# Kernel optimization log

Hardware: AMD Instinct MI355X
Metric: run time of the kernel (lower is better)

## Reference

```python
import jax, jax.numpy as jnp
import numpy as np

N = 6144
IN_FEATS = 512
OUT_FEATS = 64
NHEADS = 8
ALPHA = 0.2
NEG_BIG = -9e15


def setup_inputs() -> dict:
    key = jax.random.key(0)
    k_x, k_adj, k_w, k_a1, k_a2 = jax.random.split(key, 5)
    x = jax.random.normal(k_x, (N, IN_FEATS), dtype=jnp.float32)
    adj = jax.random.randint(k_adj, (N, N), 0, 2, dtype=jnp.int32)
    # xavier_uniform with gain=1.414 ~ sqrt(2)
    gain = 1.414
    bw = gain * np.sqrt(6.0 / (IN_FEATS + OUT_FEATS))
    W = jax.random.uniform(k_w, (NHEADS, IN_FEATS, OUT_FEATS), jnp.float32, -bw, bw)
    ba = gain * np.sqrt(6.0 / (OUT_FEATS + 1))
    a1 = jax.random.uniform(k_a1, (NHEADS, OUT_FEATS), jnp.float32, -ba, ba)
    a2 = jax.random.uniform(k_a2, (NHEADS, OUT_FEATS), jnp.float32, -ba, ba)
    return {"x": x, "adj": adj, "W": W, "a1": a1, "a2": a2}


def reference(x, adj, W, a1, a2):
    # h: [H, N, F] per-head projected features
    h = jnp.einsum("ni,hif->hnf", x, W)
    s1 = jnp.einsum("hnf,hf->hn", h, a1)  # [H, N]
    s2 = jnp.einsum("hnf,hf->hn", h, a2)  # [H, N]
    # outer-sum score [H, N, N], leaky-relu, adjacency mask, row softmax
    scores = jax.nn.leaky_relu(s1[:, :, None] + s2[:, None, :], negative_slope=ALPHA)
    scores = jnp.where(adj[None] > 0, scores, NEG_BIG)
    att = jax.nn.softmax(scores, axis=-1)
    out = jnp.einsum("hnm,hmf->hnf", att, h)  # [H, N, F]
    # concat heads: [N, H*F]
    out = jnp.transpose(out, (1, 0, 2)).reshape(N, NHEADS * OUT_FEATS)
    return jax.nn.elu(out)
```

## Files before the change

### kernel.cpp

```cpp
#include <hip/hip_runtime.h>
#include <hip/hip_bf16.h>
#include <stdint.h>

#define N_NODES 6144
#define IN_F    512
#define OUT_F   64
#define NH      8
#define ALPHA   0.2f
#define L2E     1.4426950408889634f
#define NTILES  (N_NODES / 64)

typedef __attribute__((ext_vector_type(8))) short bf16x8;
typedef __attribute__((ext_vector_type(8))) _Float16 f16x8;
typedef __attribute__((ext_vector_type(4))) float f32x4;

#define MFMA16B(a, b, c) __builtin_amdgcn_mfma_f32_16x16x32_bf16(a, b, c, 0, 0, 0)
#define MFMA16H(a, b, c) __builtin_amdgcn_mfma_f32_16x16x32_f16(a, b, c, 0, 0, 0)

__device__ __forceinline__ unsigned short f2bf(float f) {
    uint32_t u = __float_as_uint(f);
    u += 0x7fffu + ((u >> 16) & 1u);
    return (unsigned short)(u >> 16);
}
__device__ __forceinline__ float bf2f(unsigned short h) {
    return __uint_as_float(((uint32_t)h) << 16);
}
__device__ __forceinline__ unsigned short f16b(float f) {
    union { _Float16 h; unsigned short u; } c;
    c.h = (_Float16)f;
    return c.u;
}
__device__ __forceinline__ uint32_t encf(float x) {
    int i = __float_as_int(x);
    return (i >= 0) ? ((uint32_t)i | 0x80000000u) : ~(uint32_t)i;
}
__device__ __forceinline__ float decf(uint32_t u) {
    int i = (u & 0x80000000u) ? (int)(u & 0x7FFFFFFFu) : ~(int)u;
    return __int_as_float(i);
}

__global__ __launch_bounds__(256) void k_prep(
    const float* __restrict__ x, unsigned short* __restrict__ xh,
    unsigned short* __restrict__ xl,
    const float* __restrict__ W, unsigned short* __restrict__ wthF,
    unsigned short* __restrict__ wtlF, uint32_t* __restrict__ s2mu,
    const int* __restrict__ adj, unsigned long long* __restrict__ bmT)
{
    const int bid = blockIdx.x;
    if (bid < 2048) {
        const int stride = 2048 * 256;
        for (int idx = bid * 256 + threadIdx.x; idx < N_NODES * N_NODES;
             idx += stride) {
            unsigned long long b = __ballot(adj[idx] > 0);
            if ((threadIdx.x & 63) == 0) {
                int r = idx / N_NODES;
                int cb = (idx % N_NODES) >> 6;
                bmT[(size_t)cb * N_NODES + r] = b;
            }
        }
    } else if (bid < 5120) {
        int i = (bid - 2048) * 256 + threadIdx.x;
        float4 v = ((const float4*)x)[i];
        float vv[4] = {v.x, v.y, v.z, v.w};
        unsigned short h4[4], l4[4];
#pragma unroll
        for (int c = 0; c < 4; ++c) {
            unsigned short hb = f2bf(vv[c]);
            h4[c] = hb;
            l4[c] = f2bf(vv[c] - bf2f(hb));
        }
        ((ushort4*)xh)[i] = make_ushort4(h4[0], h4[1], h4[2], h4[3]);
        ((ushort4*)xl)[i] = make_ushort4(l4[0], l4[1], l4[2], l4[3]);
    } else {
        int tid = (bid - 5120) * 256 + threadIdx.x;
        if (bid == 5120 && threadIdx.x < NH) s2mu[threadIdx.x] = 0u;
        int lane = tid & 63;
        int rest = tid >> 6;
        int ct = rest & 3;
        int i = (rest >> 2) & 15;
        int h = rest >> 6;
        int f = ct * 16 + (lane & 15);
        int k0 = i * 32 + (lane >> 4) * 8;
        unsigned short oh[8], ol[8];
#pragma unroll
        for (int e = 0; e < 8; ++e) {
            float wv = W[((size_t)h * IN_F + k0 + e) * OUT_F + f];
            unsigned short hb = f2bf(wv);
            oh[e] = hb;
            ol[e] = f2bf(wv - bf2f(hb));
        }
        ushort4* dh = (ushort4*)(wthF + (size_t)tid * 8);
        dh[0] = make_ushort4(oh[0], oh[1], oh[2], oh[3]);
        dh[1] = make_ushort4(oh[4], oh[5], oh[6], oh[7]);
        ushort4* dl = (ushort4*)(wtlF + (size_t)tid * 8);
        dl[0] = make_ushort4(ol[0], ol[1], ol[2], ol[3]);
        dl[1] = make_ushort4(ol[4], ol[5], ol[6], ol[7]);
    }
}

__global__ __launch_bounds__(256) void k_proj(
    const unsigned short* __restrict__ xh, const unsigned short* __restrict__ xl,
    const unsigned short* __restrict__ wthF, const unsigned short* __restrict__ wtlF,
    const float* __restrict__ a1, const float* __restrict__ a2,
    float* __restrict__ s1, float* __restrict__ s2,
    uint32_t* __restrict__ s2mu, unsigned short* __restrict__ hTF)
{
    __shared__ unsigned short hlds[64][64];

    const int head = blockIdx.x & 7;
    const int rb = blockIdx.x >> 3;
    const int w = threadIdx.x >> 6;
    const int lane = threadIdx.x & 63;
    const int r15 = lane & 15;
    const int g = lane >> 4;
    const int rowbase = rb * 64 + w * 16;
    const int rowA = rowbase + r15;

    f32x4 acc[4] = {};
    const unsigned short* xhp = xh + (size_t)rowA * IN_F + g * 8;
    const unsigned short* xlp = xl + (size_t)rowA * IN_F + g * 8;
    const unsigned short* wb = wthF + ((size_t)head * 16 * 4 * 64) * 8 + lane * 8;
    const unsigned short* wl = wtlF + ((size_t)head * 16 * 4 * 64) * 8 + lane * 8;

#pragma unroll 4
    for (int i = 0; i < 16; ++i) {
        const int k0 = i * 32;
        bf16x8 ah = *(const bf16x8*)(xhp + k0);
        bf16x8 al = *(const bf16x8*)(xlp + k0);
#pragma unroll
        for (int ct = 0; ct < 4; ++ct) {
            const size_t fo = (size_t)(i * 4 + ct) * 512;
            bf16x8 bh = *(const bf16x8*)(wb + fo);
            bf16x8 bl = *(const bf16x8*)(wl + fo);
            acc[ct] = MFMA16B(ah, bh, acc[ct]);
            acc[ct] = MFMA16B(ah, bl, acc[ct]);
            acc[ct] = MFMA16B(al, bh, acc[ct]);
        }
    }

    float a1v[4], a2v[4];
#pragma unroll
    for (int ct = 0; ct < 4; ++ct) {
        a1v[ct] = a1[head * 64 + ct * 16 + r15];
        a2v[ct] = a2[head * 64 + ct * 16 + r15];
    }
    float sp1[4] = {0, 0, 0, 0}, sp2[4] = {0, 0, 0, 0};
#pragma unroll
    for (int ct = 0; ct < 4; ++ct)
#pragma unroll
        for (int j = 0; j < 4; ++j) {
            sp1[j] += acc[ct][j] * a1v[ct];
            sp2[j] += acc[ct][j] * a2v[ct];
        }
#pragma unroll
    for (int d = 1; d < 16; d <<= 1) {
#pragma unroll
        for (int j = 0; j < 4; ++j) {
            sp1[j] += __shfl_xor(sp1[j], d);
            sp2[j] += __shfl_xor(sp2[j], d);
        }
    }
    if (r15 == 0) {
#pragma unroll
        for (int j = 0; j < 4; ++j) {
            int n = rowbase + g * 4 + j;
            s1[head * N_NODES + n] = sp1[j];
            s2[head * N_NODES + n] = sp2[j];
        }
    }
    {
        float m = fmaxf(fmaxf(sp2[0], sp2[1]), fmaxf(sp2[2], sp2[3]));
        m = fmaxf(m, __shfl_xor(m, 16));
        m = fmaxf(m, __shfl_xor(m, 32));
        if (lane == 0) atomicMax(s2mu + head, encf(m));
    }

#pragma unroll
    for (int ct = 0; ct < 4; ++ct) {
        ushort4 pk;
        pk.x = f16b(acc[ct][0]);
        pk.y = f16b(acc[ct][1]);
        pk.z = f16b(acc[ct][2]);
        pk.w = f16b(acc[ct][3]);
        int f_l = ct * 16 + r15;
        int n0 = w * 16 + g * 4;
        int col = (((n0 >> 3) ^ (f_l & 7)) << 3) + (n0 & 7);
        *(ushort4*)&hlds[f_l][col] = pk;
    }
    __syncthreads();

#pragma unroll
    for (int q = 0; q < 2; ++q) {
        int fid = 2 * w + q;
        int wk = fid >> 2, ct = fid & 3;
        int f_l = ct * 16 + (lane & 15);
        int nch = wk * 4 + (lane >> 4);
        int col = ((nch ^ (f_l & 7)) << 3);
        int4 v = *(const int4*)&hlds[f_l][col];
        size_t base = (((size_t)(head * 96 + rb)) * 8 + fid) * 512 + lane * 8;
        *(int4*)(hTF + base) = v;
    }
}

__device__ __forceinline__ f16x8 mk_pa16(int4 ep, int4 en, uint32_t e1p2,
                                         uint32_t e1n2, uint32_t ms)
{
    const uint32_t epw[4] = {(uint32_t)ep.x, (uint32_t)ep.y, (uint32_t)ep.z,
                             (uint32_t)ep.w};
    const uint32_t enw[4] = {(uint32_t)en.x, (uint32_t)en.y, (uint32_t)en.z,
                             (uint32_t)en.w};
    union { uint32_t u[4]; f16x8 v; } r;
#define PAIR(J, B0, B1)                                                       \
    {                                                                         \
        uint32_t pa, pb, pm;                                                  \
        asm("v_pk_mul_f16 %0, %1, %2" : "=v"(pa) : "v"(e1p2), "v"(epw[J]));   \
        asm("v_pk_mul_f16 %0, %1, %2" : "=v"(pb) : "v"(e1n2), "v"(enw[J]));   \
        asm("v_pk_max_f16 %0, %1, %2" : "=v"(pm) : "v"(pa), "v"(pb));         \
        uint32_t mb0, mb1;                                                    \
        asm("v_bfe_i32 %0, %1, " #B0 ", 1" : "=v"(mb0) : "v"(ms));            \
        asm("v_bfe_i32 %0, %1, " #B1 ", 1" : "=v"(mb1) : "v"(ms));            \
        r.u[J] = pm & ((mb0 & 0x0000FFFFu) | (mb1 & 0xFFFF0000u));            \
    }
    PAIR(0, 0, 1)
    PAIR(1, 2, 3)
    PAIR(2, 4, 5)
    PAIR(3, 6, 7)
#undef PAIR
    return r.v;
}

struct Pf {
    int4 hb0, hb1, hb2, hb3;
    uint32_t m0, m1;
};

__device__ __forceinline__ f16x8 as_f16x8(int4 v) {
    union { int4 i; f16x8 h; } c;
    c.i = v;
    return c.h;
}

__global__ __launch_bounds__(256, 3) void k_flash(
    const unsigned short* __restrict__ hTF, const float* __restrict__ s1,
    const float* __restrict__ s2, const uint32_t* __restrict__ s2mu,
    const uint32_t* __restrict__ bmT32, float* __restrict__ out)
{
    __shared__ uint32_t epL[3072];
    __shared__ uint32_t enL[3072];
    __shared__ float fs[128 * 20];

    const int head = blockIdx.x & 7;
    const int rb = blockIdx.x >> 3;
    const int tid = threadIdx.x;
    const int w = tid >> 6, lane = tid & 63, r15 = lane & 15, g = lane >> 4;
    const int w01 = w & 1;
    const int wk = w >> 1;
    const int shg = g * 8;

    const float s2mh = decf(s2mu[head]);
    {
        const float4* s2h = (const float4*)(s2 + head * N_NODES);
#pragma unroll
        for (int i0 = 0; i0 < 6; ++i0) {
            int i = tid + i0 * 256;
            float4 v = s2h[i];
            uint32_t p0 = f16b(exp2f((v.x - s2mh) * L2E));
            uint32_t p1 = f16b(exp2f((v.y - s2mh) * L2E));
            uint32_t p2 = f16b(exp2f((v.z - s2mh) * L2E));
            uint32_t p3 = f16b(exp2f((v.w - s2mh) * L2E));
            uint32_t n0 = f16b(exp2f(ALPHA * (v.x - s2mh) * L2E));
            uint32_t n1 = f16b(exp2f(ALPHA * (v.y - s2mh) * L2E));
            uint32_t n2 = f16b(exp2f(ALPHA * (v.z - s2mh) * L2E));
            uint32_t n3 = f16b(exp2f(ALPHA * (v.w - s2mh) * L2E));
            epL[2 * i] = p0 | (p1 << 16);
            epL[2 * i + 1] = p2 | (p3 << 16);
            enL[2 * i] = n0 | (n1 << 16);
            enL[2 * i + 1] = n2 | (n3 << 16);
        }
    }

    const int rA = rb * 64 + w01 * 32 + r15;
    const int rB = rA + 16;
    const float s1A = s1[head * N_NODES + rA];
    const float s1B = s1[head * N_NODES + rB];
    const float t0A = s1A + s2mh, t0B = s1B + s2mh;
    const float MrA = fmaxf(t0A, ALPHA * t0A);
    const float MrB = fmaxf(t0B, ALPHA * t0B);
    uint32_t E1pA2, E1nA2, E1pB2, E1nB2;
    {
        uint32_t a = f16b(exp2f((t0A - MrA) * L2E));
        uint32_t b = f16b(exp2f((ALPHA * t0A - MrA) * L2E));
        uint32_t c = f16b(exp2f((t0B - MrB) * L2E));
        uint32_t d = f16b(exp2f((ALPHA * t0B - MrB) * L2E));
        E1pA2 = a | (a << 16);
        E1nA2 = b | (b << 16);
        E1pB2 = c | (c << 16);
        E1nB2 = d | (d << 16);
    }

    const unsigned short* __restrict__ hbp =
        hTF + ((size_t)(head * 96) * 8 + wk * 4) * 512 + lane * 8;
    const uint32_t* __restrict__ epb = epL + wk * 16 + g * 4;
    const uint32_t* __restrict__ enb = enL + wk * 16 + g * 4;
    const uint32_t* __restrict__ bmA = bmT32 + (size_t)rA * 2 + wk;
    const uint32_t* __restrict__ bmB = bmT32 + (size_t)rB * 2 + wk;

    f32x4 accA[4] = {}, accB[4] = {};
    f32x4 accSA = {}, accSB = {};
    const f16x8 vones = {(_Float16)1.0f, (_Float16)1.0f, (_Float16)1.0f,
                         (_Float16)1.0f, (_Float16)1.0f, (_Float16)1.0f,
                         (_Float16)1.0f, (_Float16)1.0f};

    __syncthreads();

    auto loadPf = [&](int t, Pf& P) {
        const unsigned short* hp = hbp + (size_t)t * 4096;
        asm volatile("global_load_dwordx4 %0, %1, off"
                     : "=v"(P.hb0) : "v"(hp));
        asm volatile("global_load_dwordx4 %0, %1, off offset:1024"
                     : "=v"(P.hb1) : "v"(hp));
        asm volatile("global_load_dwordx4 %0, %1, off offset:2048"
                     : "=v"(P.hb2) : "v"(hp));
        asm volatile("global_load_dwordx4 %0, %1, off offset:3072"
                     : "=v"(P.hb3) : "v"(hp));
        const uint32_t* pa = bmA + (size_t)t * 12288;
        const uint32_t* pb = bmB + (size_t)t * 12288;
        asm volatile("global_load_dword %0, %1, off" : "=v"(P.m0) : "v"(pa));
        asm volatile("global_load_dword %0, %1, off" : "=v"(P.m1) : "v"(pb));
    };
    auto compute = [&](int t, Pf& C) {
        int4 ep = *(const int4*)(epb + t * 32);
        int4 en = *(const int4*)(enb + t * 32);
        f16x8 paA = mk_pa16(ep, en, E1pA2, E1nA2, C.m0 >> shg);
        f16x8 paB = mk_pa16(ep, en, E1pB2, E1nB2, C.m1 >> shg);
        __builtin_amdgcn_s_setprio(1);
        accSA = MFMA16H(paA, vones, accSA);
        accSB = MFMA16H(paB, vones, accSB);
        f16x8 h0 = as_f16x8(C.hb0), h1 = as_f16x8(C.hb1);
        f16x8 h2 = as_f16x8(C.hb2), h3 = as_f16x8(C.hb3);
        accA[0] = MFMA16H(paA, h0, accA[0]);
        accB[0] = MFMA16H(paB, h0, accB[0]);
        accA[1] = MFMA16H(paA, h1, accA[1]);
        accB[1] = MFMA16H(paB, h1, accB[1]);
        accA[2] = MFMA16H(paA, h2, accA[2]);
        accB[2] = MFMA16H(paB, h2, accB[2]);
        accA[3] = MFMA16H(paA, h3, accA[3]);
        accB[3] = MFMA16H(paB, h3, accB[3]);
        __builtin_amdgcn_s_setprio(0);
    };

    Pf P0, P1, P2;
    loadPf(0, P0);
    loadPf(1, P1);
    loadPf(2, P2);
    for (int t = 0; t < NTILES; t += 3) {
        asm volatile("s_waitcnt vmcnt(12)");
        __builtin_amdgcn_sched_barrier(0);
        compute(t, P0);
        loadPf(t + 3 < NTILES ? t + 3 : NTILES - 1, P0);

        asm volatile("s_waitcnt vmcnt(12)");
        __builtin_amdgcn_sched_barrier(0);
        compute(t + 1, P1);
        loadPf(t + 4 < NTILES ? t + 4 : NTILES - 1, P1);

        asm volatile("s_waitcnt vmcnt(12)");
        __builtin_amdgcn_sched_barrier(0);
        compute(t + 2, P2);
        loadPf(t + 5 < NTILES ? t + 5 : NTILES - 1, P2);
    }
    asm volatile("s_waitcnt vmcnt(0)");
    __builtin_amdgcn_sched_barrier(0);

    const int slot = w01 * 64 + lane;
    const int fcb = head * 64;
    const int nA = rb * 64 + w01 * 32 + g * 4;

    if (wk == 1) {
#pragma unroll
        for (int ct = 0; ct < 4; ++ct)
#pragma unroll
            for (int j = 0; j < 4; ++j) fs[slot * 20 + ct * 4 + j] = accA[ct][j];
#pragma unroll
        for (int j = 0; j < 4; ++j) fs[slot * 20 + 16 + j] = accSA[j];
    }
    __syncthreads();
    if (wk == 0) {
        float rinv[4];
#pragma unroll
        for (int j = 0; j < 4; ++j)
            rinv[j] = 1.0f / (accSA[j] + fs[slot * 20 + 16 + j]);
#pragma unroll
        for (int ct = 0; ct < 4; ++ct)
#pragma unroll
            for (int j = 0; j < 4; ++j) {
                float v = (accA[ct][j] + fs[slot * 20 + ct * 4 + j]) * rinv[j];
                v = (v > 0.f) ? v : (expf(v) - 1.f);
                out[(size_t)(nA + j) * 512 + fcb + ct * 16 + r15] = v;
            }
    }
    __syncthreads();
    if (wk == 1) {
#pragma unroll
        for (int ct = 0; ct < 4; ++ct)
#pragma unroll
            for (int j = 0; j < 4; ++j) fs[slot * 20 + ct * 4 + j] = accB[ct][j];
#pragma unroll
        for (int j = 0; j < 4; ++j) fs[slot * 20 + 16 + j] = accSB[j];
    }
    __syncthreads();
    if (wk == 0) {
        float rinv[4];
#pragma unroll
        for (int j = 0; j < 4; ++j)
            rinv[j] = 1.0f / (accSB[j] + fs[slot * 20 + 16 + j]);
#pragma unroll
        for (int ct = 0; ct < 4; ++ct)
#pragma unroll
            for (int j = 0; j < 4; ++j) {
                float v = (accB[ct][j] + fs[slot * 20 + ct * 4 + j]) * rinv[j];
                v = (v > 0.f) ? v : (expf(v) - 1.f);
                out[(size_t)(nA + 16 + j) * 512 + fcb + ct * 16 + r15] = v;
            }
    }
}

extern "C" void kernel_launch(void* const* d_in, const int* in_sizes, int n_in,
                              void* d_out, int out_size, void* d_ws, size_t ws_size,
                              hipStream_t stream)
{
    const float* x = (const float*)d_in[0];
    const int* adj = (const int*)d_in[1];
    const float* W = (const float*)d_in[2];
    const float* a1 = (const float*)d_in[3];
    const float* a2 = (const float*)d_in[4];
    float* out = (float*)d_out;

    char* ws = (char*)d_ws;
    size_t off = 0;
    auto take = [&](size_t bytes) {
        void* p = ws + off;
        off = (off + bytes + 255) & ~(size_t)255;
        return p;
    };
    unsigned short* xh   = (unsigned short*)take((size_t)N_NODES * IN_F * 2);
    unsigned short* xl   = (unsigned short*)take((size_t)N_NODES * IN_F * 2);
    unsigned short* wthF = (unsigned short*)take((size_t)512 * 512 * 2);
    unsigned short* wtlF = (unsigned short*)take((size_t)512 * 512 * 2);
    unsigned short* hTF  = (unsigned short*)take((size_t)NH * 64 * N_NODES * 2);
    float* s1  = (float*)take((size_t)NH * N_NODES * 4);
    float* s2  = (float*)take((size_t)NH * N_NODES * 4);
    uint32_t* s2mu = (uint32_t*)take(256);
    unsigned long long* bmT =
        (unsigned long long*)take((size_t)N_NODES * (N_NODES / 64) * 8);

    k_prep<<<dim3(5248), dim3(256), 0, stream>>>(
        x, xh, xl, W, wthF, wtlF, s2mu, adj, bmT);
    k_proj<<<dim3(NH * (N_NODES / 64)), dim3(256), 0, stream>>>(
        xh, xl, wthF, wtlF, a1, a2, s1, s2, s2mu, hTF);
    k_flash<<<dim3(NH * NTILES), dim3(256), 0, stream>>>(
        hTF, s1, s2, s2mu, (const uint32_t*)bmT, out);
}
```

Baseline: 165.9 us.

## Transpose adjacency bitmask per wave and simplify flash prefetch addressing

The adjacency bit-packing now has each wave process a 64x64 block. It ballots 64 rows, keeps its own row's mask, and writes 64 bitmask words in one coalesced store instead of one scattered store per ballot. The flash loop's prefetch pointers now advance incrementally, the second mask load uses an immediate offset, and the tail clamp is dropped. Prefetches past the end are absorbed by padding added to the workspace buffers. The mask combine in mk_pa16 uses a single v_bfi_b32 instead of separate and/or operations.

After: 157.8 us. -4.9%, faster.

```diff
diff --git a/kernel.cpp b/kernel.cpp
--- a/kernel.cpp
+++ b/kernel.cpp
@@ -48,15 +48,17 @@
 {
     const int bid = blockIdx.x;
     if (bid < 2048) {
-        const int stride = 2048 * 256;
-        for (int idx = bid * 256 + threadIdx.x; idx < N_NODES * N_NODES;
-             idx += stride) {
-            unsigned long long b = __ballot(adj[idx] > 0);
-            if ((threadIdx.x & 63) == 0) {
-                int r = idx / N_NODES;
-                int cb = (idx % N_NODES) >> 6;
-                bmT[(size_t)cb * N_NODES + r] = b;
+        const int lane = threadIdx.x & 63;
+        const int wgid = bid * 4 + (threadIdx.x >> 6);
+        for (int ch = wgid; ch < 96 * 96; ch += 8192) {
+            const int cb = ch % 96, rblk = ch / 96;
+            const int* ap = adj + (size_t)(rblk * 64) * N_NODES + cb * 64 + lane;
+            unsigned long long keep = 0;
+            for (int rr = 0; rr < 64; ++rr) {
+                unsigned long long b = __ballot(ap[(size_t)rr * N_NODES] > 0);
+                if (lane == rr) keep = b;
             }
+            bmT[(size_t)cb * N_NODES + rblk * 64 + lane] = keep;
         }
     } else if (bid < 5120) {
         int i = (bid - 2048) * 256 + threadIdx.x;
@@ -203,7 +205,8 @@
 }
 
 __device__ __forceinline__ f16x8 mk_pa16(int4 ep, int4 en, uint32_t e1p2,
-                                         uint32_t e1n2, uint32_t ms)
+                                         uint32_t e1n2, uint32_t ms,
+                                         uint32_t kFFFF)
 {
     const uint32_t epw[4] = {(uint32_t)ep.x, (uint32_t)ep.y, (uint32_t)ep.z,
                              (uint32_t)ep.w};
@@ -212,14 +215,16 @@
     union { uint32_t u[4]; f16x8 v; } r;
 #define PAIR(J, B0, B1)                                                       \
     {                                                                         \
-        uint32_t pa, pb, pm;                                                  \
+        uint32_t pa, pb, pm, mw;                                              \
         asm("v_pk_mul_f16 %0, %1, %2" : "=v"(pa) : "v"(e1p2), "v"(epw[J]));   \
         asm("v_pk_mul_f16 %0, %1, %2" : "=v"(pb) : "v"(e1n2), "v"(enw[J]));   \
         asm("v_pk_max_f16 %0, %1, %2" : "=v"(pm) : "v"(pa), "v"(pb));         \
         uint32_t mb0, mb1;                                                    \
         asm("v_bfe_i32 %0, %1, " #B0 ", 1" : "=v"(mb0) : "v"(ms));            \
         asm("v_bfe_i32 %0, %1, " #B1 ", 1" : "=v"(mb1) : "v"(ms));            \
-        r.u[J] = pm & ((mb0 & 0x0000FFFFu) | (mb1 & 0xFFFF0000u));            \
+        asm("v_bfi_b32 %0, %1, %2, %3"                                        \
+            : "=v"(mw) : "s"(kFFFF), "v"(mb0), "v"(mb1));                     \
+        r.u[J] = pm & mw;                                                     \
     }
     PAIR(0, 0, 1)
     PAIR(1, 2, 3)
@@ -256,6 +261,7 @@
     const int w01 = w & 1;
     const int wk = w >> 1;
     const int shg = g * 8;
+    const uint32_t kFFFF = 0xFFFFu;
 
     const float s2mh = decf(s2mu[head]);
     {
@@ -298,12 +304,12 @@
         E1nB2 = d | (d << 16);
     }
 
-    const unsigned short* __restrict__ hbp =
-        hTF + ((size_t)(head * 96) * 8 + wk * 4) * 512 + lane * 8;
+    const unsigned short* hp = hTF +
+        ((size_t)(head * 96) * 8 + wk * 4) * 512 + lane * 8;
+    const uint32_t* pa = bmT32 + (size_t)rA * 2 + wk;
+
     const uint32_t* __restrict__ epb = epL + wk * 16 + g * 4;
     const uint32_t* __restrict__ enb = enL + wk * 16 + g * 4;
-    const uint32_t* __restrict__ bmA = bmT32 + (size_t)rA * 2 + wk;
-    const uint32_t* __restrict__ bmB = bmT32 + (size_t)rB * 2 + wk;
 
     f32x4 accA[4] = {}, accB[4] = {};
     f32x4 accSA = {}, accSB = {};
@@ -313,8 +319,7 @@
 
     __syncthreads();
 
-    auto loadPf = [&](int t, Pf& P) {
-        const unsigned short* hp = hbp + (size_t)t * 4096;
+    auto loadPf = [&](Pf& P) {
         asm volatile("global_load_dwordx4 %0, %1, off"
                      : "=v"(P.hb0) : "v"(hp));
         asm volatile("global_load_dwordx4 %0, %1, off offset:1024"
@@ -323,16 +328,18 @@
                      : "=v"(P.hb2) : "v"(hp));
         asm volatile("global_load_dwordx4 %0, %1, off offset:3072"
                      : "=v"(P.hb3) : "v"(hp));
-        const uint32_t* pa = bmA + (size_t)t * 12288;
-        const uint32_t* pb = bmB + (size_t)t * 12288;
-        asm volatile("global_load_dword %0, %1, off" : "=v"(P.m0) : "v"(pa));
-        asm volatile("global_load_dword %0, %1, off" : "=v"(P.m1) : "v"(pb));
+        asm volatile("global_load_dword %0, %1, off"
+                     : "=v"(P.m0) : "v"(pa));
+        asm volatile("global_load_dword %0, %1, off offset:128"
+                     : "=v"(P.m1) : "v"(pa));
+        hp += 4096;
+        pa += 12288;
     };
     auto compute = [&](int t, Pf& C) {
         int4 ep = *(const int4*)(epb + t * 32);
         int4 en = *(const int4*)(enb + t * 32);
-        f16x8 paA = mk_pa16(ep, en, E1pA2, E1nA2, C.m0 >> shg);
-        f16x8 paB = mk_pa16(ep, en, E1pB2, E1nB2, C.m1 >> shg);
+        f16x8 paA = mk_pa16(ep, en, E1pA2, E1nA2, C.m0 >> shg, kFFFF);
+        f16x8 paB = mk_pa16(ep, en, E1pB2, E1nB2, C.m1 >> shg, kFFFF);
         __builtin_amdgcn_s_setprio(1);
         accSA = MFMA16H(paA, vones, accSA);
         accSB = MFMA16H(paB, vones, accSB);
@@ -350,24 +357,24 @@
     };
 
     Pf P0, P1, P2;
-    loadPf(0, P0);
-    loadPf(1, P1);
-    loadPf(2, P2);
+    loadPf(P0);
+    loadPf(P1);
+    loadPf(P2);
     for (int t = 0; t < NTILES; t += 3) {
         asm volatile("s_waitcnt vmcnt(12)");
         __builtin_amdgcn_sched_barrier(0);
         compute(t, P0);
-        loadPf(t + 3 < NTILES ? t + 3 : NTILES - 1, P0);
+        loadPf(P0);
 
         asm volatile("s_waitcnt vmcnt(12)");
         __builtin_amdgcn_sched_barrier(0);
         compute(t + 1, P1);
-        loadPf(t + 4 < NTILES ? t + 4 : NTILES - 1, P1);
+        loadPf(P1);
 
         asm volatile("s_waitcnt vmcnt(12)");
         __builtin_amdgcn_sched_barrier(0);
         compute(t + 2, P2);
-        loadPf(t + 5 < NTILES ? t + 5 : NTILES - 1, P2);
+        loadPf(P2);
     }
     asm volatile("s_waitcnt vmcnt(0)");
     __builtin_amdgcn_sched_barrier(0);
@@ -447,12 +454,13 @@
     unsigned short* xl   = (unsigned short*)take((size_t)N_NODES * IN_F * 2);
     unsigned short* wthF = (unsigned short*)take((size_t)512 * 512 * 2);
     unsigned short* wtlF = (unsigned short*)take((size_t)512 * 512 * 2);
-    unsigned short* hTF  = (unsigned short*)take((size_t)NH * 64 * N_NODES * 2);
+    unsigned short* hTF  = (unsigned short*)take(
+        (size_t)NH * 64 * N_NODES * 2 + 32768);
     float* s1  = (float*)take((size_t)NH * N_NODES * 4);
     float* s2  = (float*)take((size_t)NH * N_NODES * 4);
     uint32_t* s2mu = (uint32_t*)take(256);
-    unsigned long long* bmT =
-        (unsigned long long*)take((size_t)N_NODES * (N_NODES / 64) * 8);
+    unsigned long long* bmT = (unsigned long long*)take(
+        (size_t)N_NODES * (N_NODES / 64) * 8 + 196608);
 
     k_prep<<<dim3(5248), dim3(256), 0, stream>>>(
         x, xh, xl, W, wthF, wtlF, s2mu, adj, bmT);
```
